# Optimization experiments

Measured on AMD Instinct MI355X. Metric: run time of the kernel, lower is better.

The kernel has to match this reference:

```python
import jax, jax.numpy as jnp
import numpy as np

B, N = 4, 65536
NUM_GROUP, GROUP_SIZE = 512, 64
EMB = 60


def setup_inputs() -> dict:
    key = jax.random.key(0)
    ks = jax.random.split(key, 8)
    inp = {
        'xyz': jax.random.uniform(ks[0], (B, N, 3), jnp.float32),
        'color': jax.random.uniform(ks[1], (B, N, 3), jnp.float32),
        'W1': jax.random.normal(ks[2], (6, 64), jnp.float32) * 0.2,
        'b1': jnp.zeros((64,), jnp.float32),
        'W2': jax.random.normal(ks[3], (64, 128), jnp.float32) * 0.1,
        'b2': jnp.zeros((128,), jnp.float32),
        'W3': jax.random.normal(ks[4], (128, 256), jnp.float32) * 0.08,
        'b3': jnp.zeros((256,), jnp.float32),
        'W4': jax.random.normal(ks[5], (256, 512), jnp.float32) * 0.06,
        'b4': jnp.zeros((512,), jnp.float32),
        'Wp': jax.random.normal(ks[6], (512, EMB), jnp.float32) * 0.04,
        'bp': jnp.zeros((EMB,), jnp.float32),
    }
    return inp


def fps(xyz, n):
    """Farthest point sampling. xyz: (B,N,3) -> centers (B,n,3)."""
    b, npts, _ = xyz.shape
    start = jnp.zeros((b,), jnp.int32)
    d0 = jnp.full((b, npts), 1e10, xyz.dtype)

    def step(carry, _):
        dists, last = carry
        p = jnp.take_along_axis(xyz, last[:, None, None], axis=1)  # (B,1,3)
        d = jnp.sum((xyz - p) ** 2, axis=-1)                       # (B,N)
        dists = jnp.minimum(dists, d)
        nxt = jnp.argmax(dists, axis=-1).astype(jnp.int32)
        return (dists, nxt), nxt

    (_, _), rest = jax.lax.scan(step, (d0, start), None, length=n - 1)
    idx = jnp.concatenate([start[:, None], rest.T], axis=1)        # (B,n)
    return jax.vmap(lambda pts, i: pts[i])(xyz, idx)


def knn_idx(k, xyz, new_xyz):
    """Indices of k nearest points in xyz for each query in new_xyz.
    xyz: (B,N,3), new_xyz: (B,S,3) -> (B,S,k) int32. Matches
    square_distance + topk(largest=False)."""
    sq = (jnp.sum(new_xyz ** 2, -1)[..., None]
          + jnp.sum(xyz ** 2, -1)[:, None, :]
          - 2.0 * jnp.einsum('bsc,bnc->bsn', new_xyz, xyz))        # (B,S,N)
    _, idx = jax.lax.top_k(-sq, k)
    return idx


def reference(xyz, color, W1, b1, W2, b2, W3, b3, W4, b4, Wp, bp):
    # --- Group: FPS centers + KNN neighborhood gather + centering ---
    center = fps(xyz, NUM_GROUP)                                   # (B,G,3)
    idx = knn_idx(GROUP_SIZE, xyz, center)                         # (B,G,M)
    gather = jax.vmap(lambda pts, i: pts[i])                       # pts[(B,)N,3], i (G,M)
    neighborhood = gather(xyz, idx) - center[:, :, None, :]        # (B,G,M,3) centered
    neighborhood_color = gather(color, idx)                        # (B,G,M,3)
    feats = jnp.concatenate([neighborhood, neighborhood_color], -1)  # (B,G,M,6)

    # --- PointNet: per-point MLP -> max over group -> projection ---
    x = jax.nn.relu(feats @ W1 + b1)
    x = jax.nn.relu(x @ W2 + b2)
    x = jax.nn.relu(x @ W3 + b3)
    x = jax.nn.relu(x @ W4 + b4)                                   # (B,G,M,512)
    x = jnp.max(x, axis=2)                                         # (B,G,512)
    emb = x @ Wp + bp                                              # (B,G,60)
    return emb, center
```

## Files before the change

### kernel.cpp

```cpp
#include <hip/hip_runtime.h>
#include <stdint.h>

#define DI __device__ __forceinline__

typedef _Float16 f16x8 __attribute__((ext_vector_type(8)));
typedef float f32x4 __attribute__((ext_vector_type(4)));

constexpr int kB = 4;
constexpr int kN = 65536;
constexpr int kG = 512;
constexpr int kM = 64;
constexpr int kE = 60;
constexpr int GRD = 20;
constexpr int NCELL = GRD * GRD * GRD;
constexpr float CW = 1.0f / 20.0f;

constexpr int FPS_SUB = 16;
constexpr int FPS_PT_T = kN / FPS_SUB / 1024;

constexpr size_t OFF_FKEY   = 0;
constexpr size_t OFF_CCNT   = OFF_FKEY + (size_t)kB * kG * FPS_SUB * 4 * 8;
constexpr size_t ZERO_BYTES = OFF_CCNT + (size_t)kB * NCELL * 4;
constexpr size_t OFF_CSTART = (ZERO_BYTES + 255) & ~(size_t)255;
constexpr size_t OFF_CUR    = OFF_CSTART + (size_t)kB * (NCELL + 1) * 4;
constexpr size_t OFF_SW1    = ((OFF_CUR + (size_t)kB * NCELL * 4) + 255) & ~(size_t)255;
constexpr size_t OFF_SW2    = OFF_SW1 + 2048 * 2;
constexpr size_t OFF_SW3    = OFF_SW2 + 8192 * 2;
constexpr size_t OFF_SW4    = OFF_SW3 + 32768 * 2;
constexpr size_t OFF_WPT    = OFF_SW4 + 131072 * 2;
constexpr size_t OFF_SORT   = ((OFF_WPT + 60 * 512 * 4) + 255) & ~(size_t)255;
constexpr size_t OFF_KIDX   = OFF_SORT + (size_t)kB * kN * 16;

DI int cellof(float x) {
  int c = (int)(x * (float)GRD);
  return min(GRD - 1, max(0, c));
}
DI unsigned orderable(float f) {
  unsigned u = __float_as_uint(f);
  return (u & 0x80000000u) ? ~u : (u | 0x80000000u);
}

__global__ void k_zero(uint32_t* p, int nwords) {
  int i = blockIdx.x * blockDim.x + threadIdx.x;
  int st = gridDim.x * blockDim.x;
  for (; i < nwords; i += st) p[i] = 0u;
}

DI void swz(const float* __restrict__ W, _Float16* __restrict__ sw,
            int total, int nks, int Kreal, int N, int i0, int st) {
  for (int i = i0; i < total; i += st) {
    int j = i & 7, lane = (i >> 3) & 63, rest = i >> 9;
    int ks = rest % nks, nt = rest / nks;
    int k = ks * 32 + ((lane >> 4) << 3) + j;
    int n = nt * 16 + (lane & 15);
    sw[i] = (_Float16)((k < Kreal) ? W[k * N + n] : 0.f);
  }
}

__global__ void k_prep(const float* __restrict__ W1, const float* __restrict__ W2,
                       const float* __restrict__ W3, const float* __restrict__ W4,
                       const float* __restrict__ Wp,
                       _Float16* __restrict__ sw1, _Float16* __restrict__ sw2,
                       _Float16* __restrict__ sw3, _Float16* __restrict__ sw4,
                       float* __restrict__ wpt) {
  int i0 = blockIdx.x * blockDim.x + threadIdx.x;
  int st = gridDim.x * blockDim.x;
  swz(W1, sw1, 2048, 1, 6, 64, i0, st);
  swz(W2, sw2, 8192, 2, 64, 128, i0, st);
  swz(W3, sw3, 32768, 4, 128, 256, i0, st);
  swz(W4, sw4, 131072, 8, 256, 512, i0, st);
  for (int i = i0; i < 60 * 512; i += st) { int n = i >> 9, k = i & 511; wpt[i] = Wp[k * 60 + n]; }
}

__global__ __launch_bounds__(1024) void k_fps(const float* __restrict__ xyz,
                                              float* __restrict__ outC,
                                              unsigned long long* __restrict__ fkey) {
  const int b = blockIdx.x / FPS_SUB, sub = blockIdx.x % FPS_SUB;
  const int tid = threadIdx.x;
  const int wave = tid >> 6, lane = tid & 63;
  const float* X = xyz + (size_t)b * kN * 3;
  float px[FPS_PT_T], py[FPS_PT_T], pz[FPS_PT_T], dd[FPS_PT_T];
#pragma unroll
  for (int j = 0; j < FPS_PT_T; ++j) {
    int p = sub * (kN / FPS_SUB) + j * 1024 + tid;
    px[j] = X[3 * p]; py[j] = X[3 * p + 1]; pz[j] = X[3 * p + 2];
    dd[j] = 1e10f;
  }
  float lx = X[0], ly = X[1], lz = X[2];
  if (sub == 0 && tid == 0) {
    outC[(size_t)b * kG * 3 + 0] = lx;
    outC[(size_t)b * kG * 3 + 1] = ly;
    outC[(size_t)b * kG * 3 + 2] = lz;
  }
  __shared__ unsigned long long wkey[16];
  __shared__ float wx[16], wy[16], wz[16];
  __shared__ float4 sp;
  unsigned long long* keyB = fkey + (size_t)b * kG * FPS_SUB * 4;

  for (int it = 1; it < kG; ++it) {
    unsigned long long best = 0ull;
    float bx = 0.f, by = 0.f, bz = 0.f;
#pragma unroll
    for (int j = 0; j < FPS_PT_T; ++j) {
      float dx = __fsub_rn(px[j], lx);
      float dy = __fsub_rn(py[j], ly);
      float dz = __fsub_rn(pz[j], lz);
      float d = __fadd_rn(__fadd_rn(__fmul_rn(dx, dx), __fmul_rn(dy, dy)), __fmul_rn(dz, dz));
      float nd = fminf(dd[j], d);
      dd[j] = nd;
      int p = sub * (kN / FPS_SUB) + j * 1024 + tid;
      unsigned long long pk =
          ((unsigned long long)__float_as_uint(nd) << 32) | (unsigned)(0xFFFFFFFFu - (unsigned)p);
      if (pk > best) { best = pk; bx = px[j]; by = py[j]; bz = pz[j]; }
    }
#pragma unroll
    for (int off = 32; off; off >>= 1) {
      unsigned long long ok = __shfl_down(best, (unsigned)off);
      float ox = __shfl_down(bx, (unsigned)off);
      float oy = __shfl_down(by, (unsigned)off);
      float oz = __shfl_down(bz, (unsigned)off);
      if (ok > best) { best = ok; bx = ox; by = oy; bz = oz; }
    }
    if (lane == 0) { wkey[wave] = best; wx[wave] = bx; wy[wave] = by; wz[wave] = bz; }
    __syncthreads();
    if (wave == 0) {
      int i16 = lane & 15;
      unsigned long long kk = wkey[i16];
      float kx = wx[i16], ky = wy[i16], kz = wz[i16];
#pragma unroll
      for (int off = 8; off; off >>= 1) {
        unsigned long long ok = __shfl_down(kk, (unsigned)off);
        float ox = __shfl_down(kx, (unsigned)off);
        float oy = __shfl_down(ky, (unsigned)off);
        float oz = __shfl_down(kz, (unsigned)off);
        if (ok > kk) { kk = ok; kx = ox; ky = oy; kz = oz; }
      }
      unsigned long long* slots = keyB + (size_t)it * (FPS_SUB * 4);
      if (lane == 0) {
        unsigned long long tag = (unsigned)it;
        unsigned long long* my = slots + sub * 4;
        __hip_atomic_store(my + 1, ((unsigned long long)__float_as_uint(kx) << 32) | tag,
                           __ATOMIC_RELAXED, __HIP_MEMORY_SCOPE_AGENT);
        __hip_atomic_store(my + 2, ((unsigned long long)__float_as_uint(ky) << 32) | tag,
                           __ATOMIC_RELAXED, __HIP_MEMORY_SCOPE_AGENT);
        __hip_atomic_store(my + 3, ((unsigned long long)__float_as_uint(kz) << 32) | tag,
                           __ATOMIC_RELAXED, __HIP_MEMORY_SCOPE_AGENT);
        __hip_atomic_store(my + 0, kk, __ATOMIC_RELAXED, __HIP_MEMORY_SCOPE_AGENT);
      }
      unsigned long long v;
      bool ok;
      long bail = 0;
      do {
        v = __hip_atomic_load(slots + lane, __ATOMIC_RELAXED, __HIP_MEMORY_SCOPE_AGENT);
        ok = (lane & 3) ? ((unsigned)v == (unsigned)it) : (v != 0ull);
      } while (!__all(ok) && ++bail < 100000000L);
      unsigned long long key = (lane & 3) ? 0ull : v;
      int slot = lane >> 2;
#pragma unroll
      for (int off = 32; off; off >>= 1) {
        unsigned long long ok2 = __shfl_down(key, (unsigned)off);
        int os = __shfl_down(slot, (unsigned)off);
        if (ok2 > key) { key = ok2; slot = os; }
      }
      slot = __shfl(slot, 0);
      unsigned long long vx = __shfl(v, slot * 4 + 1);
      unsigned long long vy = __shfl(v, slot * 4 + 2);
      unsigned long long vz = __shfl(v, slot * 4 + 3);
      if (lane == 0) {
        float wxc = __uint_as_float((unsigned)(vx >> 32));
        float wyc = __uint_as_float((unsigned)(vy >> 32));
        float wzc = __uint_as_float((unsigned)(vz >> 32));
        sp = make_float4(wxc, wyc, wzc, 0.f);
        if (sub == 0) {
          outC[((size_t)b * kG + it) * 3 + 0] = wxc;
          outC[((size_t)b * kG + it) * 3 + 1] = wyc;
          outC[((size_t)b * kG + it) * 3 + 2] = wzc;
        }
      }
    }
    __syncthreads();
    lx = sp.x; ly = sp.y; lz = sp.z;
  }
}

__global__ void k_cellcount(const float* __restrict__ xyz, uint32_t* __restrict__ ccnt) {
  int i = blockIdx.x * blockDim.x + threadIdx.x;
  int st = gridDim.x * blockDim.x;
  for (; i < kB * kN; i += st) {
    int b = i >> 16, p = i & (kN - 1);
    const float* q = xyz + ((size_t)b * kN + p) * 3;
    int cid = (cellof(q[2]) * GRD + cellof(q[1])) * GRD + cellof(q[0]);
    atomicAdd(&ccnt[b * NCELL + cid], 1u);
  }
}

__global__ void k_scan(const uint32_t* __restrict__ ccnt, uint32_t* __restrict__ cstart,
                       uint32_t* __restrict__ cur) {
  int b = blockIdx.x, tid = threadIdx.x;
  const uint32_t* cc = ccnt + (size_t)b * NCELL;
  uint32_t* cs = cstart + (size_t)b * (NCELL + 1);
  uint32_t* cu = cur + (size_t)b * NCELL;
  __shared__ uint32_t part[256];
  const int chunk = 32;
  int c0 = tid * chunk;
  uint32_t s = 0;
  for (int i = 0; i < chunk; ++i) { int c = c0 + i; if (c < NCELL) s += cc[c]; }
  part[tid] = s;
  __syncthreads();
  for (int off = 1; off < 256; off <<= 1) {
    uint32_t add = (tid >= off) ? part[tid - off] : 0u;
    __syncthreads();
    part[tid] += add;
    __syncthreads();
  }
  uint32_t run = part[tid] - s;
  for (int i = 0; i < chunk; ++i) {
    int c = c0 + i;
    if (c < NCELL) { cs[c] = run; cu[c] = run; run += cc[c]; }
  }
  if (tid == 255) cs[NCELL] = run;
}

__global__ void k_scatter(const float* __restrict__ xyz, uint32_t* __restrict__ cur,
                          float4* __restrict__ sorted) {
  int i = blockIdx.x * blockDim.x + threadIdx.x;
  int st = gridDim.x * blockDim.x;
  for (; i < kB * kN; i += st) {
    int b = i >> 16, p = i & (kN - 1);
    const float* q = xyz + ((size_t)b * kN + p) * 3;
    float x = q[0], y = q[1], z = q[2];
    int cid = (cellof(z) * GRD + cellof(y)) * GRD + cellof(x);
    uint32_t pos = atomicAdd(&cur[b * NCELL + cid], 1u);
    sorted[(size_t)b * kN + pos] = make_float4(x, y, z, __uint_as_float((unsigned)p));
  }
}

constexpr int CAP = 8192;

DI void bitonic(unsigned long long* a, int n, int tid) {
  for (int k = 2; k <= n; k <<= 1)
    for (int j = k >> 1; j > 0; j >>= 1) {
      __syncthreads();
      for (int i = tid; i < n; i += 256) {
        int ix = i ^ j;
        if (ix > i) {
          unsigned long long x = a[i], y = a[ix];
          bool up = ((i & k) == 0);
          if ((x > y) == up) { a[i] = y; a[ix] = x; }
        }
      }
    }
  __syncthreads();
}

__global__ __launch_bounds__(256) void k_knn(const float4* __restrict__ sorted,
                                             const uint32_t* __restrict__ cstart,
                                             const float* __restrict__ outC,
                                             uint32_t* __restrict__ kidx) {
  const int bi = blockIdx.x;
  const int b = (bi & 7) >> 1;
  const int g = ((bi >> 3) << 1) | (bi & 1);
  const int tid = threadIdx.x;
  __shared__ unsigned long long cand[CAP];
  __shared__ int nC;
  const float cx = outC[((size_t)b * kG + g) * 3 + 0];
  const float cy = outC[((size_t)b * kG + g) * 3 + 1];
  const float cz = outC[((size_t)b * kG + g) * 3 + 2];
  const float nc = __fadd_rn(__fadd_rn(__fmul_rn(cx, cx), __fmul_rn(cy, cy)), __fmul_rn(cz, cz));
  const float4* SP = sorted + (size_t)b * kN;
  const uint32_t* CS = cstart + (size_t)b * (NCELL + 1);
  const int ccx = cellof(cx), ccy = cellof(cy), ccz = cellof(cz);
  if (tid == 0) nC = 0;
  __syncthreads();
  int plox = 1, phix = 0, ploy = 1, phiy = 0, ploz = 1, phiz = 0;
  for (int r = 1; r <= GRD; ++r) {
    int lox = max(0, ccx - r), hix = min(GRD - 1, ccx + r);
    int loy = max(0, ccy - r), hiy = min(GRD - 1, ccy + r);
    int loz = max(0, ccz - r), hiz = min(GRD - 1, ccz + r);
    for (int z = loz; z <= hiz; ++z)
      for (int y = loy; y <= hiy; ++y) {
        bool rowPrev = (r > 1) && (z >= ploz && z <= phiz && y >= ploy && y <= phiy);
        for (int s = 0; s < 2; ++s) {
          int xa, xb;
          if (!rowPrev) { if (s) break; xa = lox; xb = hix; }
          else if (s == 0) { xa = lox; xb = plox - 1; }
          else { xa = phix + 1; xb = hix; }
          if (xa > xb) continue;
          int c0 = (z * GRD + y) * GRD + xa;
          int i0 = CS[c0];
          int i1 = CS[(z * GRD + y) * GRD + xb + 1];
          for (int i = i0 + tid; i < i1; i += 256) {
            float4 pt = SP[i];
            float npn = __fadd_rn(__fadd_rn(__fmul_rn(pt.x, pt.x), __fmul_rn(pt.y, pt.y)),
                                  __fmul_rn(pt.z, pt.z));
            float dot = __fadd_rn(__fadd_rn(__fmul_rn(cx, pt.x), __fmul_rn(cy, pt.y)),
                                  __fmul_rn(cz, pt.z));
            float sq = __fsub_rn(__fadd_rn(nc, npn), __fmul_rn(2.0f, dot));
            unsigned key = orderable(sq);
            int pos = atomicAdd(&nC, 1);
            if (pos < CAP)
              cand[pos] = ((unsigned long long)key << 32) | (unsigned)__float_as_uint(pt.w);
          }
        }
      }
    __syncthreads();
    int n = min(nC, CAP);
    float rc = 1e30f;
    if (lox > 0) rc = fminf(rc, cx - (float)lox * CW);
    if (hix < GRD - 1) rc = fminf(rc, (float)(hix + 1) * CW - cx);
    if (loy > 0) rc = fminf(rc, cy - (float)loy * CW);
    if (hiy < GRD - 1) rc = fminf(rc, (float)(hiy + 1) * CW - cy);
    if (loz > 0) rc = fminf(rc, cz - (float)loz * CW);
    if (hiz < GRD - 1) rc = fminf(rc, (float)(hiz + 1) * CW - cz);
    float r2 = (rc >= 1e29f) ? 3.0e38f : rc * rc * (1.0f - 1e-5f);
    unsigned keyR = orderable(r2);
    bool done = false;
    if (n >= kM) {
      int np2 = 1;
      while (np2 < n) np2 <<= 1;
      for (int i = n + tid; i < np2; i += 256) cand[i] = ~0ull;
      bitonic(cand, np2, tid);
      unsigned k63 = (unsigned)(cand[kM - 1] >> 32);
      done = (k63 <= keyR);
      if (tid == 0) nC = n;
    }
    __syncthreads();
    if (done) break;
    plox = lox; phix = hix; ploy = loy; phiy = hiy; ploz = loz; phiz = hiz;
  }
  if (tid < kM)
    kidx[((size_t)b * kG + g) * kM + tid] = (uint32_t)(cand[tid] & 0xFFFFFFFFu);
}


template <int Kdim, int Ndim, int SIN, int SOUT>
DI void mfma_layer(const _Float16* __restrict__ Xin, _Float16* __restrict__ Xout,
                   const _Float16* __restrict__ Wsw, const float* __restrict__ bias,
                   int wave, int lane) {
  constexpr int NKS = Kdim / 32;
  constexpr int NTW = Ndim / 64;
  constexpr int CH = (NTW < 4) ? NTW : 4;
  const int quad = lane >> 4, l16 = lane & 15;
  for (int c0 = 0; c0 < NTW; c0 += CH) {
    f32x4 acc[CH][4];
#pragma unroll
    for (int nt = 0; nt < CH; ++nt) {
      float bv = bias[wave * (Ndim / 4) + (c0 + nt) * 16 + l16];
#pragma unroll
      for (int m = 0; m < 4; ++m) acc[nt][m] = {bv, bv, bv, bv};
    }
#pragma unroll
    for (int ks = 0; ks < NKS; ++ks) {
      f16x8 af[4];
#pragma unroll
      for (int m = 0; m < 4; ++m)
        af[m] = *(const f16x8*)(Xin + (m * 16 + l16) * SIN + ks * 32 + quad * 8);
#pragma unroll
      for (int nt = 0; nt < CH; ++nt) {
        int ntg = wave * NTW + c0 + nt;
        f16x8 bf = *(const f16x8*)(Wsw + ((size_t)(ntg * NKS + ks) * 64 + lane) * 8);
#pragma unroll
        for (int m = 0; m < 4; ++m)
          acc[nt][m] = __builtin_amdgcn_mfma_f32_16x16x32_f16(af[m], bf, acc[nt][m], 0, 0, 0);
      }
    }
#pragma unroll
    for (int nt = 0; nt < CH; ++nt) {
      int col = wave * (Ndim / 4) + (c0 + nt) * 16 + l16;
#pragma unroll
      for (int m = 0; m < 4; ++m)
#pragma unroll
        for (int r = 0; r < 4; ++r) {
          int row = m * 16 + quad * 4 + r;
          Xout[row * SOUT + col] = (_Float16)fmaxf(acc[nt][m][r], 0.f);
        }
    }
  }
}

DI void mfma_layer4(const _Float16* __restrict__ Xin, const _Float16* __restrict__ Wsw,
                    const float* __restrict__ bias, float* __restrict__ maxv,
                    int wave, int lane) {
  constexpr int SIN = 264, NKS = 8, NTW = 8, CH = 4;
  const int quad = lane >> 4, l16 = lane & 15;
  for (int c0 = 0; c0 < NTW; c0 += CH) {
    f32x4 acc[CH][4];
#pragma unroll
    for (int nt = 0; nt < CH; ++nt) {
      float bv = bias[wave * 128 + (c0 + nt) * 16 + l16];
#pragma unroll
      for (int m = 0; m < 4; ++m) acc[nt][m] = {bv, bv, bv, bv};
    }
#pragma unroll
    for (int ks = 0; ks < NKS; ++ks) {
      f16x8 af[4];
#pragma unroll
      for (int m = 0; m < 4; ++m)
        af[m] = *(const f16x8*)(Xin + (m * 16 + l16) * SIN + ks * 32 + quad * 8);
#pragma unroll
      for (int nt = 0; nt < CH; ++nt) {
        int ntg = wave * NTW + c0 + nt;
        f16x8 bf = *(const f16x8*)(Wsw + ((size_t)(ntg * NKS + ks) * 64 + lane) * 8);
#pragma unroll
        for (int m = 0; m < 4; ++m)
          acc[nt][m] = __builtin_amdgcn_mfma_f32_16x16x32_f16(af[m], bf, acc[nt][m], 0, 0, 0);
      }
    }
#pragma unroll
    for (int nt = 0; nt < CH; ++nt) {
      float mx = 0.f;
#pragma unroll
      for (int m = 0; m < 4; ++m)
#pragma unroll
        for (int r = 0; r < 4; ++r) mx = fmaxf(mx, acc[nt][m][r]);
      mx = fmaxf(mx, __shfl_xor(mx, 16, 64));
      mx = fmaxf(mx, __shfl_xor(mx, 32, 64));
      if (quad == 0) maxv[wave * 128 + (c0 + nt) * 16 + l16] = mx;
    }
  }
}

__global__ __launch_bounds__(256) void k_mlp(
    const float* __restrict__ xyz, const float* __restrict__ color,
    const float* __restrict__ outC, const uint32_t* __restrict__ kidx,
    const _Float16* __restrict__ sw1, const _Float16* __restrict__ sw2,
    const _Float16* __restrict__ sw3, const _Float16* __restrict__ sw4,
    const float* __restrict__ wpt,
    const float* __restrict__ b1, const float* __restrict__ b2,
    const float* __restrict__ b3, const float* __restrict__ b4,
    const float* __restrict__ bp, float* __restrict__ outE) {
  const int bi = blockIdx.x;
  const int b = (bi & 7) >> 1;
  const int g = ((bi >> 3) << 1) | (bi & 1);
  const int tid = threadIdx.x;
  const int wave = tid >> 6, lane = tid & 63;
  __shared__ __align__(16) char smem[17408 + 33792];
  _Float16* bufA = (_Float16*)smem;
  _Float16* bufB = (_Float16*)(smem + 17408);
  float* maxv = (float*)smem;
  float* psum = (float*)(smem + 2048);

  if (tid < kM) {
    uint32_t p = kidx[((size_t)b * kG + g) * kM + tid];
    const float* cen = outC + ((size_t)b * kG + g) * 3;
    const float* xp = xyz + ((size_t)b * kN + p) * 3;
    const float* cp = color + ((size_t)b * kN + p) * 3;
    f16x8 v = {};
    v[0] = (_Float16)__fsub_rn(xp[0], cen[0]);
    v[1] = (_Float16)__fsub_rn(xp[1], cen[1]);
    v[2] = (_Float16)__fsub_rn(xp[2], cen[2]);
    v[3] = (_Float16)cp[0];
    v[4] = (_Float16)cp[1];
    v[5] = (_Float16)cp[2];
    f16x8 z = {};
    *(f16x8*)(bufA + tid * 40 + 0) = v;
    *(f16x8*)(bufA + tid * 40 + 8) = z;
    *(f16x8*)(bufA + tid * 40 + 16) = z;
    *(f16x8*)(bufA + tid * 40 + 24) = z;
  }
  __syncthreads();
  mfma_layer<32, 64, 40, 72>(bufA, bufB, sw1, b1, wave, lane);
  __syncthreads();
  mfma_layer<64, 128, 72, 136>(bufB, bufA, sw2, b2, wave, lane);
  __syncthreads();
  mfma_layer<128, 256, 136, 264>(bufA, bufB, sw3, b3, wave, lane);
  __syncthreads();
  mfma_layer4(bufB, sw4, b4, maxv, wave, lane);
  __syncthreads();
  if (tid < 240) {
    int j = tid >> 2, q = tid & 3;
    const float* w = wpt + (size_t)j * 512 + q * 128;
    float s = 0.f;
#pragma unroll 4
    for (int k = 0; k < 128; ++k) s = fmaf(maxv[q * 128 + k], w[k], s);
    psum[tid] = s;
  }
  __syncthreads();
  if (tid < kE) {
    float e = __fadd_rn(__fadd_rn(psum[tid * 4 + 0], psum[tid * 4 + 1]),
                        __fadd_rn(psum[tid * 4 + 2], psum[tid * 4 + 3])) + bp[tid];
    outE[((size_t)b * kG + g) * kE + tid] = e;
  }
}

extern "C" void kernel_launch(void* const* d_in, const int* in_sizes, int n_in,
                              void* d_out, int out_size, void* d_ws, size_t ws_size,
                              hipStream_t stream) {
  (void)in_sizes; (void)n_in; (void)out_size; (void)ws_size;
  const float* xyz = (const float*)d_in[0];
  const float* color = (const float*)d_in[1];
  const float* W1 = (const float*)d_in[2];
  const float* b1 = (const float*)d_in[3];
  const float* W2 = (const float*)d_in[4];
  const float* b2 = (const float*)d_in[5];
  const float* W3 = (const float*)d_in[6];
  const float* b3 = (const float*)d_in[7];
  const float* W4 = (const float*)d_in[8];
  const float* b4 = (const float*)d_in[9];
  const float* Wp = (const float*)d_in[10];
  const float* bp = (const float*)d_in[11];

  char* ws = (char*)d_ws;
  auto fkey = (unsigned long long*)(ws + OFF_FKEY);
  auto ccnt = (uint32_t*)(ws + OFF_CCNT);
  auto cstart = (uint32_t*)(ws + OFF_CSTART);
  auto cur = (uint32_t*)(ws + OFF_CUR);
  auto sw1 = (_Float16*)(ws + OFF_SW1);
  auto sw2 = (_Float16*)(ws + OFF_SW2);
  auto sw3 = (_Float16*)(ws + OFF_SW3);
  auto sw4 = (_Float16*)(ws + OFF_SW4);
  auto wpt = (float*)(ws + OFF_WPT);
  auto sorted = (float4*)(ws + OFF_SORT);
  auto kidx = (uint32_t*)(ws + OFF_KIDX);

  float* outE = (float*)d_out;
  float* outC = outE + (size_t)kB * kG * kE;

  k_zero<<<128, 256, 0, stream>>>((uint32_t*)ws, (int)(ZERO_BYTES / 4));
  k_prep<<<256, 256, 0, stream>>>(W1, W2, W3, W4, Wp, sw1, sw2, sw3, sw4, wpt);
  k_fps<<<kB * FPS_SUB, 1024, 0, stream>>>(xyz, outC, fkey);
  k_cellcount<<<512, 256, 0, stream>>>(xyz, ccnt);
  k_scan<<<kB, 256, 0, stream>>>(ccnt, cstart, cur);
  k_scatter<<<512, 256, 0, stream>>>(xyz, cur, sorted);
  k_knn<<<kB * kG, 256, 0, stream>>>(sorted, cstart, outC, kidx);
  k_mlp<<<kB * kG, 256, 0, stream>>>(xyz, color, outC, kidx, sw1, sw2, sw3, sw4, wpt,
                                     b1, b2, b3, b4, bp, outE);
}
```

Measured before the change: 2.257 ms.

## Fuse FPS, grid build, KNN and MLP into one persistent kernel overlapping FPS

Merges the FPS, cell count, scan, scatter, KNN and MLP kernels into a single persistent launch. 32 blocks run FPS, now with 8 sub-blocks of 256 threads, while 448 worker blocks build the spatial grid behind software global barriers. The workers then consume each FPS center as soon as it is published and run KNN plus the MLP for that group. This hides the grid build and the per-group work behind the serial FPS loop and removes the kidx round-trip through memory. The risks are that correctness depends on all blocks being co-resident for the spin barriers, and FPS now has fewer threads per point set.

```diff
diff --git a/kernel.cpp b/kernel.cpp
--- a/kernel.cpp
+++ b/kernel.cpp
@@ -5,6 +5,7 @@
 
 typedef _Float16 f16x8 __attribute__((ext_vector_type(8)));
 typedef float f32x4 __attribute__((ext_vector_type(4)));
+typedef unsigned long long u64;
 
 constexpr int kB = 4;
 constexpr int kN = 65536;
@@ -15,12 +16,17 @@
 constexpr int NCELL = GRD * GRD * GRD;
 constexpr float CW = 1.0f / 20.0f;
 
-constexpr int FPS_SUB = 16;
-constexpr int FPS_PT_T = kN / FPS_SUB / 1024;
+constexpr int FPS_SUB = 8;
+constexpr int FPS_TPB = 256;
+constexpr int FPS_PT_T = kN / FPS_SUB / FPS_TPB;
+constexpr int NFPS = kB * FPS_SUB;
+constexpr int NWORK = 448;
+constexpr int NBLK = NFPS + NWORK;
 
 constexpr size_t OFF_FKEY   = 0;
 constexpr size_t OFF_CCNT   = OFF_FKEY + (size_t)kB * kG * FPS_SUB * 4 * 8;
-constexpr size_t ZERO_BYTES = OFF_CCNT + (size_t)kB * NCELL * 4;
+constexpr size_t OFF_GS     = OFF_CCNT + (size_t)kB * NCELL * 4;
+constexpr size_t ZERO_BYTES = OFF_GS + 64;
 constexpr size_t OFF_CSTART = (ZERO_BYTES + 255) & ~(size_t)255;
 constexpr size_t OFF_CUR    = OFF_CSTART + (size_t)kB * (NCELL + 1) * 4;
 constexpr size_t OFF_SW1    = ((OFF_CUR + (size_t)kB * NCELL * 4) + 255) & ~(size_t)255;
@@ -29,7 +35,6 @@
 constexpr size_t OFF_SW4    = OFF_SW3 + 32768 * 2;
 constexpr size_t OFF_WPT    = OFF_SW4 + 131072 * 2;
 constexpr size_t OFF_SORT   = ((OFF_WPT + 60 * 512 * 4) + 255) & ~(size_t)255;
-constexpr size_t OFF_KIDX   = OFF_SORT + (size_t)kB * kN * 16;
 
 DI int cellof(float x) {
   int c = (int)(x * (float)GRD);
@@ -72,17 +77,29 @@
   for (int i = i0; i < 60 * 512; i += st) { int n = i >> 9, k = i & 511; wpt[i] = Wp[k * 60 + n]; }
 }
 
-__global__ __launch_bounds__(1024) void k_fps(const float* __restrict__ xyz,
-                                              float* __restrict__ outC,
-                                              unsigned long long* __restrict__ fkey) {
-  const int b = blockIdx.x / FPS_SUB, sub = blockIdx.x % FPS_SUB;
+DI void gbar(uint32_t* ctr, unsigned target) {
+  __syncthreads();
+  if (threadIdx.x == 0) {
+    __hip_atomic_fetch_add(ctr, 1u, __ATOMIC_ACQ_REL, __HIP_MEMORY_SCOPE_AGENT);
+    long bail = 0;
+    while (__hip_atomic_load(ctr, __ATOMIC_ACQUIRE, __HIP_MEMORY_SCOPE_AGENT) < target) {
+      __builtin_amdgcn_s_sleep(32);
+      if (++bail > 100000000L) break;
+    }
+  }
+  __syncthreads();
+}
+
+DI void fps_block(const float* __restrict__ xyz, float* __restrict__ outC,
+                  u64* __restrict__ fkey, int bi) {
+  const int b = bi / FPS_SUB, sub = bi % FPS_SUB;
   const int tid = threadIdx.x;
   const int wave = tid >> 6, lane = tid & 63;
   const float* X = xyz + (size_t)b * kN * 3;
   float px[FPS_PT_T], py[FPS_PT_T], pz[FPS_PT_T], dd[FPS_PT_T];
 #pragma unroll
   for (int j = 0; j < FPS_PT_T; ++j) {
-    int p = sub * (kN / FPS_SUB) + j * 1024 + tid;
+    int p = sub * (kN / FPS_SUB) + j * FPS_TPB + tid;
     px[j] = X[3 * p]; py[j] = X[3 * p + 1]; pz[j] = X[3 * p + 2];
     dd[j] = 1e10f;
   }
@@ -92,14 +109,14 @@
     outC[(size_t)b * kG * 3 + 1] = ly;
     outC[(size_t)b * kG * 3 + 2] = lz;
   }
-  __shared__ unsigned long long wkey[16];
-  __shared__ float wx[16], wy[16], wz[16];
+  __shared__ u64 s_key[4];
+  __shared__ float s_x[4], s_y[4], s_z[4];
   __shared__ float4 sp;
-  unsigned long long* keyB = fkey + (size_t)b * kG * FPS_SUB * 4;
+  u64* keyB = fkey + (size_t)b * kG * (FPS_SUB * 4);
 
   for (int it = 1; it < kG; ++it) {
-    unsigned long long best = 0ull;
-    float bx = 0.f, by = 0.f, bz = 0.f;
+    float bnd = -1.0f, bx = 0.f, by = 0.f, bz = 0.f;
+    int bp = 0;
 #pragma unroll
     for (int j = 0; j < FPS_PT_T; ++j) {
       float dx = __fsub_rn(px[j], lx);
@@ -108,64 +125,62 @@
       float d = __fadd_rn(__fadd_rn(__fmul_rn(dx, dx), __fmul_rn(dy, dy)), __fmul_rn(dz, dz));
       float nd = fminf(dd[j], d);
       dd[j] = nd;
-      int p = sub * (kN / FPS_SUB) + j * 1024 + tid;
-      unsigned long long pk =
-          ((unsigned long long)__float_as_uint(nd) << 32) | (unsigned)(0xFFFFFFFFu - (unsigned)p);
-      if (pk > best) { best = pk; bx = px[j]; by = py[j]; bz = pz[j]; }
-    }
+      int p = sub * (kN / FPS_SUB) + j * FPS_TPB + tid;
+      if (nd > bnd) { bnd = nd; bx = px[j]; by = py[j]; bz = pz[j]; bp = p; }
+    }
+    u64 best = ((u64)__float_as_uint(bnd) << 32) | (unsigned)(0xFFFFFFFFu - (unsigned)bp);
 #pragma unroll
     for (int off = 32; off; off >>= 1) {
-      unsigned long long ok = __shfl_down(best, (unsigned)off);
+      u64 ok = __shfl_down(best, (unsigned)off);
       float ox = __shfl_down(bx, (unsigned)off);
       float oy = __shfl_down(by, (unsigned)off);
       float oz = __shfl_down(bz, (unsigned)off);
       if (ok > best) { best = ok; bx = ox; by = oy; bz = oz; }
     }
-    if (lane == 0) { wkey[wave] = best; wx[wave] = bx; wy[wave] = by; wz[wave] = bz; }
+    if (lane == 0) { s_key[wave] = best; s_x[wave] = bx; s_y[wave] = by; s_z[wave] = bz; }
     __syncthreads();
     if (wave == 0) {
-      int i16 = lane & 15;
-      unsigned long long kk = wkey[i16];
-      float kx = wx[i16], ky = wy[i16], kz = wz[i16];
-#pragma unroll
-      for (int off = 8; off; off >>= 1) {
-        unsigned long long ok = __shfl_down(kk, (unsigned)off);
+      int i4 = lane & 3;
+      u64 kk = s_key[i4]; float kx = s_x[i4], ky = s_y[i4], kz = s_z[i4];
+#pragma unroll
+      for (int off = 2; off; off >>= 1) {
+        u64 ok = __shfl_down(kk, (unsigned)off);
         float ox = __shfl_down(kx, (unsigned)off);
         float oy = __shfl_down(ky, (unsigned)off);
         float oz = __shfl_down(kz, (unsigned)off);
         if (ok > kk) { kk = ok; kx = ox; ky = oy; kz = oz; }
       }
-      unsigned long long* slots = keyB + (size_t)it * (FPS_SUB * 4);
+      u64* slots = keyB + (size_t)it * (FPS_SUB * 4);
       if (lane == 0) {
-        unsigned long long tag = (unsigned)it;
-        unsigned long long* my = slots + sub * 4;
-        __hip_atomic_store(my + 1, ((unsigned long long)__float_as_uint(kx) << 32) | tag,
+        u64 tag = (unsigned)it;
+        u64* my = slots + sub * 4;
+        __hip_atomic_store(my + 1, ((u64)__float_as_uint(kx) << 32) | tag,
                            __ATOMIC_RELAXED, __HIP_MEMORY_SCOPE_AGENT);
-        __hip_atomic_store(my + 2, ((unsigned long long)__float_as_uint(ky) << 32) | tag,
+        __hip_atomic_store(my + 2, ((u64)__float_as_uint(ky) << 32) | tag,
                            __ATOMIC_RELAXED, __HIP_MEMORY_SCOPE_AGENT);
-        __hip_atomic_store(my + 3, ((unsigned long long)__float_as_uint(kz) << 32) | tag,
+        __hip_atomic_store(my + 3, ((u64)__float_as_uint(kz) << 32) | tag,
                            __ATOMIC_RELAXED, __HIP_MEMORY_SCOPE_AGENT);
         __hip_atomic_store(my + 0, kk, __ATOMIC_RELAXED, __HIP_MEMORY_SCOPE_AGENT);
       }
-      unsigned long long v;
-      bool ok;
-      long bail = 0;
+      u64 v = 0; bool okp; long bail = 0;
       do {
-        v = __hip_atomic_load(slots + lane, __ATOMIC_RELAXED, __HIP_MEMORY_SCOPE_AGENT);
-        ok = (lane & 3) ? ((unsigned)v == (unsigned)it) : (v != 0ull);
-      } while (!__all(ok) && ++bail < 100000000L);
-      unsigned long long key = (lane & 3) ? 0ull : v;
+        if (lane < FPS_SUB * 4)
+          v = __hip_atomic_load(slots + lane, __ATOMIC_RELAXED, __HIP_MEMORY_SCOPE_AGENT);
+        okp = (lane >= FPS_SUB * 4) ||
+              ((lane & 3) ? ((unsigned)v == (unsigned)it) : (v != 0ull));
+      } while (!__all(okp) && ++bail < 200000000L);
+      u64 key = (lane < FPS_SUB * 4 && (lane & 3) == 0) ? v : 0ull;
       int slot = lane >> 2;
 #pragma unroll
-      for (int off = 32; off; off >>= 1) {
-        unsigned long long ok2 = __shfl_down(key, (unsigned)off);
+      for (int off = 16; off >= 4; off >>= 1) {
+        u64 ok = __shfl_down(key, (unsigned)off);
         int os = __shfl_down(slot, (unsigned)off);
-        if (ok2 > key) { key = ok2; slot = os; }
+        if (ok > key) { key = ok; slot = os; }
       }
       slot = __shfl(slot, 0);
-      unsigned long long vx = __shfl(v, slot * 4 + 1);
-      unsigned long long vy = __shfl(v, slot * 4 + 2);
-      unsigned long long vz = __shfl(v, slot * 4 + 3);
+      u64 vx = __shfl(v, slot * 4 + 1);
+      u64 vy = __shfl(v, slot * 4 + 2);
+      u64 vz = __shfl(v, slot * 4 + 3);
       if (lane == 0) {
         float wxc = __uint_as_float((unsigned)(vx >> 32));
         float wyc = __uint_as_float((unsigned)(vy >> 32));
@@ -183,68 +198,14 @@
   }
 }
 
-__global__ void k_cellcount(const float* __restrict__ xyz, uint32_t* __restrict__ ccnt) {
-  int i = blockIdx.x * blockDim.x + threadIdx.x;
-  int st = gridDim.x * blockDim.x;
-  for (; i < kB * kN; i += st) {
-    int b = i >> 16, p = i & (kN - 1);
-    const float* q = xyz + ((size_t)b * kN + p) * 3;
-    int cid = (cellof(q[2]) * GRD + cellof(q[1])) * GRD + cellof(q[0]);
-    atomicAdd(&ccnt[b * NCELL + cid], 1u);
-  }
-}
-
-__global__ void k_scan(const uint32_t* __restrict__ ccnt, uint32_t* __restrict__ cstart,
-                       uint32_t* __restrict__ cur) {
-  int b = blockIdx.x, tid = threadIdx.x;
-  const uint32_t* cc = ccnt + (size_t)b * NCELL;
-  uint32_t* cs = cstart + (size_t)b * (NCELL + 1);
-  uint32_t* cu = cur + (size_t)b * NCELL;
-  __shared__ uint32_t part[256];
-  const int chunk = 32;
-  int c0 = tid * chunk;
-  uint32_t s = 0;
-  for (int i = 0; i < chunk; ++i) { int c = c0 + i; if (c < NCELL) s += cc[c]; }
-  part[tid] = s;
-  __syncthreads();
-  for (int off = 1; off < 256; off <<= 1) {
-    uint32_t add = (tid >= off) ? part[tid - off] : 0u;
-    __syncthreads();
-    part[tid] += add;
-    __syncthreads();
-  }
-  uint32_t run = part[tid] - s;
-  for (int i = 0; i < chunk; ++i) {
-    int c = c0 + i;
-    if (c < NCELL) { cs[c] = run; cu[c] = run; run += cc[c]; }
-  }
-  if (tid == 255) cs[NCELL] = run;
-}
-
-__global__ void k_scatter(const float* __restrict__ xyz, uint32_t* __restrict__ cur,
-                          float4* __restrict__ sorted) {
-  int i = blockIdx.x * blockDim.x + threadIdx.x;
-  int st = gridDim.x * blockDim.x;
-  for (; i < kB * kN; i += st) {
-    int b = i >> 16, p = i & (kN - 1);
-    const float* q = xyz + ((size_t)b * kN + p) * 3;
-    float x = q[0], y = q[1], z = q[2];
-    int cid = (cellof(z) * GRD + cellof(y)) * GRD + cellof(x);
-    uint32_t pos = atomicAdd(&cur[b * NCELL + cid], 1u);
-    sorted[(size_t)b * kN + pos] = make_float4(x, y, z, __uint_as_float((unsigned)p));
-  }
-}
-
-constexpr int CAP = 8192;
-
-DI void bitonic(unsigned long long* a, int n, int tid) {
+DI void bitonic(u64* a, int n, int tid) {
   for (int k = 2; k <= n; k <<= 1)
     for (int j = k >> 1; j > 0; j >>= 1) {
       __syncthreads();
       for (int i = tid; i < n; i += 256) {
         int ix = i ^ j;
         if (ix > i) {
-          unsigned long long x = a[i], y = a[ix];
+          u64 x = a[i], y = a[ix];
           bool up = ((i & k) == 0);
           if ((x > y) == up) { a[i] = y; a[ix] = x; }
         }
@@ -252,86 +213,6 @@
     }
   __syncthreads();
 }
-
-__global__ __launch_bounds__(256) void k_knn(const float4* __restrict__ sorted,
-                                             const uint32_t* __restrict__ cstart,
-                                             const float* __restrict__ outC,
-                                             uint32_t* __restrict__ kidx) {
-  const int bi = blockIdx.x;
-  const int b = (bi & 7) >> 1;
-  const int g = ((bi >> 3) << 1) | (bi & 1);
-  const int tid = threadIdx.x;
-  __shared__ unsigned long long cand[CAP];
-  __shared__ int nC;
-  const float cx = outC[((size_t)b * kG + g) * 3 + 0];
-  const float cy = outC[((size_t)b * kG + g) * 3 + 1];
-  const float cz = outC[((size_t)b * kG + g) * 3 + 2];
-  const float nc = __fadd_rn(__fadd_rn(__fmul_rn(cx, cx), __fmul_rn(cy, cy)), __fmul_rn(cz, cz));
-  const float4* SP = sorted + (size_t)b * kN;
-  const uint32_t* CS = cstart + (size_t)b * (NCELL + 1);
-  const int ccx = cellof(cx), ccy = cellof(cy), ccz = cellof(cz);
-  if (tid == 0) nC = 0;
-  __syncthreads();
-  int plox = 1, phix = 0, ploy = 1, phiy = 0, ploz = 1, phiz = 0;
-  for (int r = 1; r <= GRD; ++r) {
-    int lox = max(0, ccx - r), hix = min(GRD - 1, ccx + r);
-    int loy = max(0, ccy - r), hiy = min(GRD - 1, ccy + r);
-    int loz = max(0, ccz - r), hiz = min(GRD - 1, ccz + r);
-    for (int z = loz; z <= hiz; ++z)
-      for (int y = loy; y <= hiy; ++y) {
-        bool rowPrev = (r > 1) && (z >= ploz && z <= phiz && y >= ploy && y <= phiy);
-        for (int s = 0; s < 2; ++s) {
-          int xa, xb;
-          if (!rowPrev) { if (s) break; xa = lox; xb = hix; }
-          else if (s == 0) { xa = lox; xb = plox - 1; }
-          else { xa = phix + 1; xb = hix; }
-          if (xa > xb) continue;
-          int c0 = (z * GRD + y) * GRD + xa;
-          int i0 = CS[c0];
-          int i1 = CS[(z * GRD + y) * GRD + xb + 1];
-          for (int i = i0 + tid; i < i1; i += 256) {
-            float4 pt = SP[i];
-            float npn = __fadd_rn(__fadd_rn(__fmul_rn(pt.x, pt.x), __fmul_rn(pt.y, pt.y)),
-                                  __fmul_rn(pt.z, pt.z));
-            float dot = __fadd_rn(__fadd_rn(__fmul_rn(cx, pt.x), __fmul_rn(cy, pt.y)),
-                                  __fmul_rn(cz, pt.z));
-            float sq = __fsub_rn(__fadd_rn(nc, npn), __fmul_rn(2.0f, dot));
-            unsigned key = orderable(sq);
-            int pos = atomicAdd(&nC, 1);
-            if (pos < CAP)
-              cand[pos] = ((unsigned long long)key << 32) | (unsigned)__float_as_uint(pt.w);
-          }
-        }
-      }
-    __syncthreads();
-    int n = min(nC, CAP);
-    float rc = 1e30f;
-    if (lox > 0) rc = fminf(rc, cx - (float)lox * CW);
-    if (hix < GRD - 1) rc = fminf(rc, (float)(hix + 1) * CW - cx);
-    if (loy > 0) rc = fminf(rc, cy - (float)loy * CW);
-    if (hiy < GRD - 1) rc = fminf(rc, (float)(hiy + 1) * CW - cy);
-    if (loz > 0) rc = fminf(rc, cz - (float)loz * CW);
-    if (hiz < GRD - 1) rc = fminf(rc, (float)(hiz + 1) * CW - cz);
-    float r2 = (rc >= 1e29f) ? 3.0e38f : rc * rc * (1.0f - 1e-5f);
-    unsigned keyR = orderable(r2);
-    bool done = false;
-    if (n >= kM) {
-      int np2 = 1;
-      while (np2 < n) np2 <<= 1;
-      for (int i = n + tid; i < np2; i += 256) cand[i] = ~0ull;
-      bitonic(cand, np2, tid);
-      unsigned k63 = (unsigned)(cand[kM - 1] >> 32);
-      done = (k63 <= keyR);
-      if (tid == 0) nC = n;
-    }
-    __syncthreads();
-    if (done) break;
-    plox = lox; phix = hix; ploy = loy; phiy = hiy; ploz = loz; phiz = hiz;
-  }
-  if (tid < kM)
-    kidx[((size_t)b * kG + g) * kM + tid] = (uint32_t)(cand[tid] & 0xFFFFFFFFu);
-}
-
 
 template <int Kdim, int Ndim, int SIN, int SOUT>
 DI void mfma_layer(const _Float16* __restrict__ Xin, _Float16* __restrict__ Xout,
@@ -420,66 +301,220 @@
   }
 }
 
-__global__ __launch_bounds__(256) void k_mlp(
+__global__ __launch_bounds__(256, 2) void k_fused(
     const float* __restrict__ xyz, const float* __restrict__ color,
-    const float* __restrict__ outC, const uint32_t* __restrict__ kidx,
+    float* __restrict__ outC, float* __restrict__ outE,
+    u64* __restrict__ fkey, uint32_t* __restrict__ ccnt,
+    uint32_t* __restrict__ cstart, uint32_t* __restrict__ cur,
+    float4* __restrict__ sorted, uint32_t* __restrict__ gs,
     const _Float16* __restrict__ sw1, const _Float16* __restrict__ sw2,
     const _Float16* __restrict__ sw3, const _Float16* __restrict__ sw4,
     const float* __restrict__ wpt,
     const float* __restrict__ b1, const float* __restrict__ b2,
     const float* __restrict__ b3, const float* __restrict__ b4,
-    const float* __restrict__ bp, float* __restrict__ outE) {
+    const float* __restrict__ bp) {
   const int bi = blockIdx.x;
-  const int b = (bi & 7) >> 1;
-  const int g = ((bi >> 3) << 1) | (bi & 1);
+  if (bi < NFPS) { fps_block(xyz, outC, fkey, bi); return; }
+
+  const int wj = bi - NFPS;
   const int tid = threadIdx.x;
   const int wave = tid >> 6, lane = tid & 63;
-  __shared__ __align__(16) char smem[17408 + 33792];
-  _Float16* bufA = (_Float16*)smem;
-  _Float16* bufB = (_Float16*)(smem + 17408);
-  float* maxv = (float*)smem;
-  float* psum = (float*)(smem + 2048);
-
-  if (tid < kM) {
-    uint32_t p = kidx[((size_t)b * kG + g) * kM + tid];
-    const float* cen = outC + ((size_t)b * kG + g) * 3;
-    const float* xp = xyz + ((size_t)b * kN + p) * 3;
-    const float* cp = color + ((size_t)b * kN + p) * 3;
-    f16x8 v = {};
-    v[0] = (_Float16)__fsub_rn(xp[0], cen[0]);
-    v[1] = (_Float16)__fsub_rn(xp[1], cen[1]);
-    v[2] = (_Float16)__fsub_rn(xp[2], cen[2]);
-    v[3] = (_Float16)cp[0];
-    v[4] = (_Float16)cp[1];
-    v[5] = (_Float16)cp[2];
-    f16x8 z = {};
-    *(f16x8*)(bufA + tid * 40 + 0) = v;
-    *(f16x8*)(bufA + tid * 40 + 8) = z;
-    *(f16x8*)(bufA + tid * 40 + 16) = z;
-    *(f16x8*)(bufA + tid * 40 + 24) = z;
-  }
-  __syncthreads();
-  mfma_layer<32, 64, 40, 72>(bufA, bufB, sw1, b1, wave, lane);
-  __syncthreads();
-  mfma_layer<64, 128, 72, 136>(bufB, bufA, sw2, b2, wave, lane);
-  __syncthreads();
-  mfma_layer<128, 256, 136, 264>(bufA, bufB, sw3, b3, wave, lane);
-  __syncthreads();
-  mfma_layer4(bufB, sw4, b4, maxv, wave, lane);
-  __syncthreads();
-  if (tid < 240) {
-    int j = tid >> 2, q = tid & 3;
-    const float* w = wpt + (size_t)j * 512 + q * 128;
-    float s = 0.f;
+  __shared__ __align__(16) char smem[65536];
+  __shared__ int nC;
+  __shared__ float4 spc;
+  __shared__ uint32_t s_part[256];
+  u64* cand = (u64*)smem;
+
+  for (int i = wj * 256 + tid; i < kB * kN; i += NWORK * 256) {
+    int b = i >> 16, p = i & (kN - 1);
+    const float* q = xyz + ((size_t)b * kN + p) * 3;
+    int cid = (cellof(q[2]) * GRD + cellof(q[1])) * GRD + cellof(q[0]);
+    atomicAdd(&ccnt[b * NCELL + cid], 1u);
+  }
+  gbar(gs + 0, NWORK);
+  if (wj < kB) {
+    int b = wj;
+    const uint32_t* cc = ccnt + (size_t)b * NCELL;
+    uint32_t* cs = cstart + (size_t)b * (NCELL + 1);
+    uint32_t* cu = cur + (size_t)b * NCELL;
+    const int chunk = 32;
+    int c0 = tid * chunk;
+    uint32_t s = 0;
+    for (int i = 0; i < chunk; ++i) { int c = c0 + i; if (c < NCELL) s += cc[c]; }
+    s_part[tid] = s;
+    __syncthreads();
+    for (int off = 1; off < 256; off <<= 1) {
+      uint32_t add = (tid >= off) ? s_part[tid - off] : 0u;
+      __syncthreads();
+      s_part[tid] += add;
+      __syncthreads();
+    }
+    uint32_t run = s_part[tid] - s;
+    for (int i = 0; i < chunk; ++i) {
+      int c = c0 + i;
+      if (c < NCELL) { cs[c] = run; cu[c] = run; run += cc[c]; }
+    }
+    if (tid == 255) cs[NCELL] = run;
+  }
+  gbar(gs + 1, NWORK);
+  for (int i = wj * 256 + tid; i < kB * kN; i += NWORK * 256) {
+    int b = i >> 16, p = i & (kN - 1);
+    const float* q = xyz + ((size_t)b * kN + p) * 3;
+    float x = q[0], y = q[1], z = q[2];
+    int cid = (cellof(z) * GRD + cellof(y)) * GRD + cellof(x);
+    uint32_t pos = atomicAdd(&cur[b * NCELL + cid], 1u);
+    sorted[(size_t)b * kN + pos] = make_float4(x, y, z, __uint_as_float((unsigned)p));
+  }
+  gbar(gs + 2, NWORK);
+
+  for (int j = wj; j < kB * kG; j += NWORK) {
+    const int it = j >> 2, b = j & 3;
+    const float* X = xyz + (size_t)b * kN * 3;
+    if (it == 0) {
+      if (tid == 0) spc = make_float4(X[0], X[1], X[2], 0.f);
+    } else if (tid < 64) {
+      const u64* slots = fkey + ((size_t)b * kG + it) * (FPS_SUB * 4);
+      const int pl = tid;
+      u64 v = 0; bool okp; long bail = 0;
+      for (;;) {
+        if (pl < FPS_SUB * 4)
+          v = __hip_atomic_load(slots + pl, __ATOMIC_RELAXED, __HIP_MEMORY_SCOPE_AGENT);
+        okp = (pl >= FPS_SUB * 4) ||
+              ((pl & 3) ? ((unsigned)v == (unsigned)it) : (v != 0ull));
+        if (__all(okp)) break;
+        __builtin_amdgcn_s_sleep(127);
+        if (++bail > 50000000L) break;
+      }
+      u64 key = (pl < FPS_SUB * 4 && (pl & 3) == 0) ? v : 0ull;
+      int slot = pl >> 2;
+#pragma unroll
+      for (int off = 16; off >= 4; off >>= 1) {
+        u64 ok = __shfl_down(key, (unsigned)off);
+        int os = __shfl_down(slot, (unsigned)off);
+        if (ok > key) { key = ok; slot = os; }
+      }
+      slot = __shfl(slot, 0);
+      u64 vx = __shfl(v, slot * 4 + 1);
+      u64 vy = __shfl(v, slot * 4 + 2);
+      u64 vz = __shfl(v, slot * 4 + 3);
+      if (pl == 0)
+        spc = make_float4(__uint_as_float((unsigned)(vx >> 32)),
+                          __uint_as_float((unsigned)(vy >> 32)),
+                          __uint_as_float((unsigned)(vz >> 32)), 0.f);
+    }
+    __syncthreads();
+    const float cx = spc.x, cy = spc.y, cz = spc.z;
+
+    const float nc = __fadd_rn(__fadd_rn(__fmul_rn(cx, cx), __fmul_rn(cy, cy)), __fmul_rn(cz, cz));
+    const float4* SP = sorted + (size_t)b * kN;
+    const uint32_t* CS = cstart + (size_t)b * (NCELL + 1);
+    const int ccx = cellof(cx), ccy = cellof(cy), ccz = cellof(cz);
+    if (tid == 0) nC = 0;
+    __syncthreads();
+    int plox = 1, phix = 0, ploy = 1, phiy = 0, ploz = 1, phiz = 0;
+    for (int r = 1; r <= GRD; ++r) {
+      int lox = max(0, ccx - r), hix = min(GRD - 1, ccx + r);
+      int loy = max(0, ccy - r), hiy = min(GRD - 1, ccy + r);
+      int loz = max(0, ccz - r), hiz = min(GRD - 1, ccz + r);
+      for (int z = loz; z <= hiz; ++z)
+        for (int y = loy; y <= hiy; ++y) {
+          bool rowPrev = (r > 1) && (z >= ploz && z <= phiz && y >= ploy && y <= phiy);
+          for (int s = 0; s < 2; ++s) {
+            int xa, xb;
+            if (!rowPrev) { if (s) break; xa = lox; xb = hix; }
+            else if (s == 0) { xa = lox; xb = plox - 1; }
+            else { xa = phix + 1; xb = hix; }
+            if (xa > xb) continue;
+            int c0 = (z * GRD + y) * GRD + xa;
+            int i0 = CS[c0];
+            int i1 = CS[(z * GRD + y) * GRD + xb + 1];
+            for (int i = i0 + tid; i < i1; i += 256) {
+              float4 pt = SP[i];
+              float npn = __fadd_rn(__fadd_rn(__fmul_rn(pt.x, pt.x), __fmul_rn(pt.y, pt.y)),
+                                    __fmul_rn(pt.z, pt.z));
+              float dot = __fadd_rn(__fadd_rn(__fmul_rn(cx, pt.x), __fmul_rn(cy, pt.y)),
+                                    __fmul_rn(cz, pt.z));
+              float sq = __fsub_rn(__fadd_rn(nc, npn), __fmul_rn(2.0f, dot));
+              unsigned key = orderable(sq);
+              int pos = atomicAdd(&nC, 1);
+              if (pos < 8192)
+                cand[pos] = ((u64)key << 32) | (unsigned)__float_as_uint(pt.w);
+            }
+          }
+        }
+      __syncthreads();
+      int n = min(nC, 8192);
+      float rc = 1e30f;
+      if (lox > 0) rc = fminf(rc, cx - (float)lox * CW);
+      if (hix < GRD - 1) rc = fminf(rc, (float)(hix + 1) * CW - cx);
+      if (loy > 0) rc = fminf(rc, cy - (float)loy * CW);
+      if (hiy < GRD - 1) rc = fminf(rc, (float)(hiy + 1) * CW - cy);
+      if (loz > 0) rc = fminf(rc, cz - (float)loz * CW);
+      if (hiz < GRD - 1) rc = fminf(rc, (float)(hiz + 1) * CW - cz);
+      float r2 = (rc >= 1e29f) ? 3.0e38f : rc * rc * (1.0f - 1e-5f);
+      unsigned keyR = orderable(r2);
+      bool done = false;
+      if (n >= kM) {
+        int np2 = 1;
+        while (np2 < n) np2 <<= 1;
+        for (int i = n + tid; i < np2; i += 256) cand[i] = ~0ull;
+        bitonic(cand, np2, tid);
+        unsigned k63 = (unsigned)(cand[kM - 1] >> 32);
+        done = (k63 <= keyR);
+        if (tid == 0) nC = n;
+      }
+      __syncthreads();
+      if (done) break;
+      plox = lox; phix = hix; ploy = loy; phiy = hiy; ploz = loz; phiz = hiz;
+    }
+
+    uint32_t pidx = 0;
+    if (tid < kM) pidx = (uint32_t)(cand[tid] & 0xFFFFFFFFu);
+    __syncthreads();
+    _Float16* bufA = (_Float16*)smem;
+    _Float16* bufB = (_Float16*)(smem + 17408);
+    float* maxv = (float*)smem;
+    float* psum = (float*)(smem + 2048);
+    if (tid < kM) {
+      const float* xp = xyz + ((size_t)b * kN + pidx) * 3;
+      const float* cp = color + ((size_t)b * kN + pidx) * 3;
+      f16x8 v = {};
+      v[0] = (_Float16)__fsub_rn(xp[0], cx);
+      v[1] = (_Float16)__fsub_rn(xp[1], cy);
+      v[2] = (_Float16)__fsub_rn(xp[2], cz);
+      v[3] = (_Float16)cp[0];
+      v[4] = (_Float16)cp[1];
+      v[5] = (_Float16)cp[2];
+      f16x8 zf = {};
+      *(f16x8*)(bufA + tid * 40 + 0) = v;
+      *(f16x8*)(bufA + tid * 40 + 8) = zf;
+      *(f16x8*)(bufA + tid * 40 + 16) = zf;
+      *(f16x8*)(bufA + tid * 40 + 24) = zf;
+    }
+    __syncthreads();
+    mfma_layer<32, 64, 40, 72>(bufA, bufB, sw1, b1, wave, lane);
+    __syncthreads();
+    mfma_layer<64, 128, 72, 136>(bufB, bufA, sw2, b2, wave, lane);
+    __syncthreads();
+    mfma_layer<128, 256, 136, 264>(bufA, bufB, sw3, b3, wave, lane);
+    __syncthreads();
+    mfma_layer4(bufB, sw4, b4, maxv, wave, lane);
+    __syncthreads();
+    if (tid < 240) {
+      int jj = tid >> 2, q = tid & 3;
+      const float* w = wpt + (size_t)jj * 512 + q * 128;
+      float s = 0.f;
 #pragma unroll 4
-    for (int k = 0; k < 128; ++k) s = fmaf(maxv[q * 128 + k], w[k], s);
-    psum[tid] = s;
-  }
-  __syncthreads();
-  if (tid < kE) {
-    float e = __fadd_rn(__fadd_rn(psum[tid * 4 + 0], psum[tid * 4 + 1]),
-                        __fadd_rn(psum[tid * 4 + 2], psum[tid * 4 + 3])) + bp[tid];
-    outE[((size_t)b * kG + g) * kE + tid] = e;
+      for (int k = 0; k < 128; ++k) s = fmaf(maxv[q * 128 + k], w[k], s);
+      psum[tid] = s;
+    }
+    __syncthreads();
+    if (tid < kE) {
+      float e = __fadd_rn(__fadd_rn(psum[tid * 4 + 0], psum[tid * 4 + 1]),
+                          __fadd_rn(psum[tid * 4 + 2], psum[tid * 4 + 3])) + bp[tid];
+      outE[((size_t)b * kG + it) * kE + tid] = e;
+    }
+    __syncthreads();
   }
 }
 
@@ -501,8 +536,9 @@
   const float* bp = (const float*)d_in[11];
 
   char* ws = (char*)d_ws;
-  auto fkey = (unsigned long long*)(ws + OFF_FKEY);
+  auto fkey = (u64*)(ws + OFF_FKEY);
   auto ccnt = (uint32_t*)(ws + OFF_CCNT);
+  auto gs = (uint32_t*)(ws + OFF_GS);
   auto cstart = (uint32_t*)(ws + OFF_CSTART);
   auto cur = (uint32_t*)(ws + OFF_CUR);
   auto sw1 = (_Float16*)(ws + OFF_SW1);
@@ -511,18 +547,13 @@
   auto sw4 = (_Float16*)(ws + OFF_SW4);
   auto wpt = (float*)(ws + OFF_WPT);
   auto sorted = (float4*)(ws + OFF_SORT);
-  auto kidx = (uint32_t*)(ws + OFF_KIDX);
 
   float* outE = (float*)d_out;
   float* outC = outE + (size_t)kB * kG * kE;
 
   k_zero<<<128, 256, 0, stream>>>((uint32_t*)ws, (int)(ZERO_BYTES / 4));
   k_prep<<<256, 256, 0, stream>>>(W1, W2, W3, W4, Wp, sw1, sw2, sw3, sw4, wpt);
-  k_fps<<<kB * FPS_SUB, 1024, 0, stream>>>(xyz, outC, fkey);
-  k_cellcount<<<512, 256, 0, stream>>>(xyz, ccnt);
-  k_scan<<<kB, 256, 0, stream>>>(ccnt, cstart, cur);
-  k_scatter<<<512, 256, 0, stream>>>(xyz, cur, sorted);
-  k_knn<<<kB * kG, 256, 0, stream>>>(sorted, cstart, outC, kidx);
-  k_mlp<<<kB * kG, 256, 0, stream>>>(xyz, color, outC, kidx, sw1, sw2, sw3, sw4, wpt,
-                                     b1, b2, b3, b4, bp, outE);
-}
+  k_fused<<<NBLK, 256, 0, stream>>>(xyz, color, outC, outE, fkey, ccnt, cstart, cur,
+                                    sorted, gs, sw1, sw2, sw3, sw4, wpt,
+                                    b1, b2, b3, b4, bp);
+}
```

After: 2.128 ms. 5.7% less time.
